# Optimization experiments

Measured on AMD Instinct MI355X. Metric: run time of the kernel, lower is better.

## Reference

```python
import jax, jax.numpy as jnp
import numpy as np

B, N, D, YD = 256, 1024, 64, 2
EPS = 1e-7  # keras SCC epsilon clip


def interleave(x):
    # (B, L, ...): out[:,0::2]=first half, out[:,1::2]=second half
    b, L = x.shape[0], x.shape[1]
    a, c = x[:, : L // 2], x[:, L // 2:]
    return jnp.stack([a, c], axis=2).reshape((b, L) + x.shape[2:])


def block_interleave(x, scope):
    # tf.split into N//scope chunks of size `scope`, Interleave each, concat
    b, L = x.shape[0], x.shape[1]
    rest = x.shape[2:]
    xr = x.reshape((b, L // scope, 2, scope // 2) + rest)
    xr = jnp.swapaxes(xr, 2, 3)
    return xr.reshape((b, L) + rest)


def split_even_odd(x):
    # returns (odd, even) = (x[:,0::2], x[:,1::2])
    return x[:, 0::2], x[:, 1::2]


def mlp2(x, W1, b1, W2, b2):
    return jnp.dot(jax.nn.relu(jnp.dot(x, W1) + b1), W2) + b2


def emb2llr(e, W, b):
    return jax.nn.softmax(jnp.dot(e, W) + b, axis=-1)


def scce(v, p):
    # v: (B,L,1) int labels, p: (B,L,2) probs -> (B,L) per-element NLL
    pt = jnp.take_along_axis(p, v, axis=-1)[..., 0]
    return -jnp.log(jnp.clip(pt, EPS, 1.0))


def setup_inputs() -> dict:
    key = jax.random.key(0)
    ks = jax.random.split(key, 16)
    s = lambda fan: 1.0 / np.sqrt(fan)
    return {
        "x": jax.random.randint(ks[0], (B, N, 1), 0, 2, dtype=jnp.int32),
        "y": jax.random.normal(ks[1], (B, N, YD), dtype=jnp.float32),
        "emb_W": jax.random.normal(ks[2], (YD, D), dtype=jnp.float32) * s(YD),
        "emb_b": jnp.zeros((D,), jnp.float32),
        "lab_emb": jax.random.normal(ks[3], (2, D), dtype=jnp.float32) * s(D),
        "cn_W1": jax.random.normal(ks[4], (2 * D, D), dtype=jnp.float32) * s(2 * D),
        "cn_b1": jnp.zeros((D,), jnp.float32),
        "cn_W2": jax.random.normal(ks[5], (D, D), dtype=jnp.float32) * s(D),
        "cn_b2": jnp.zeros((D,), jnp.float32),
        "bn_W1": jax.random.normal(ks[6], (3 * D, D), dtype=jnp.float32) * s(3 * D),
        "bn_b1": jnp.zeros((D,), jnp.float32),
        "bn_W2": jax.random.normal(ks[7], (D, D), dtype=jnp.float32) * s(D),
        "bn_b2": jnp.zeros((D,), jnp.float32),
        "llr_W": jax.random.normal(ks[8], (D, 2), dtype=jnp.float32) * s(D),
        "llr_b": jnp.zeros((2,), jnp.float32),
    }


def reference(x, y, emb_W, emb_b, lab_emb, cn_W1, cn_b1, cn_W2, cn_b2,
              bn_W1, bn_b1, bn_W2, bn_b2, llr_W, llr_b):
    v = x.astype(jnp.int32)  # (B,N,1)
    e = jnp.dot(y, emb_W) + emb_b  # (B,N,D) observation embedding

    losses, preds, norms = [], [], []
    pred = emb2llr(e, llr_W, llr_b)
    losses.append(scce(v, pred))
    preds.append(pred)
    norms.append(jnp.linalg.norm(e, axis=-1))

    scope = 2
    while scope <= N:
        v_il = block_interleave(v, scope)
        v_odd, v_even = split_even_odd(v_il)
        v_xor = jnp.mod(v_odd + v_even, 2)  # (B,N/2,1)
        v_prime = interleave(jnp.concatenate((v_xor, v_even), axis=1))

        e_il = block_interleave(e, scope)
        e_odd, e_even = split_even_odd(e_il)  # (B,N/2,D) each
        v_xor_emb = lab_emb[v_xor[..., 0]]  # (B,N/2,D)

        e1_left = mlp2(jnp.concatenate((e_odd, e_even), axis=-1),
                       cn_W1, cn_b1, cn_W2, cn_b2)
        e1_right = mlp2(jnp.concatenate((e_odd, e_even, v_xor_emb), axis=-1),
                        bn_W1, bn_b1, bn_W2, bn_b2)
        e_prime = interleave(jnp.concatenate((e1_left, e1_right), axis=1))

        pred = emb2llr(e_prime, llr_W, llr_b)
        losses.append(scce(v_prime, pred))
        preds.append(pred)
        norms.append(jnp.linalg.norm(e_prime, axis=-1))

        v, e = v_prime, e_prime
        scope *= 2

    return (jnp.stack(losses, axis=-2),   # (B, S, N)
            jnp.stack(preds, axis=-2),    # (B, N, S, 2)
            jnp.stack(norms, axis=-2))    # (B, S, N)
```

## Files before the change

kernel.cpp:

```cpp
#include <hip/hip_runtime.h>
#include <hip/hip_bf16.h>

#define NB 256
#define NN 1024
#define NSTAGES 11
#define EPSF 1e-7f

typedef unsigned short u16;
typedef unsigned int u32;
typedef unsigned long long u64;
typedef __attribute__((ext_vector_type(8))) short short8;
typedef __attribute__((ext_vector_type(16))) float f32x16;

static constexpr size_t PRED_BASE = (size_t)NB * NSTAGES * NN;
static constexpr size_t NORM_BASE = PRED_BASE + (size_t)NB * NN * NSTAGES * 2;

static constexpr int LW_OFF = 24576;

#define WLDS_FR 30
#define NWREG (48 - WLDS_FR)

__device__ __forceinline__ u16 f2bf(float f) {
  unsigned u = __float_as_uint(f);
  unsigned r = (u + 0x7fffu + ((u >> 16) & 1u)) >> 16;
  return (u16)r;
}
__device__ __forceinline__ unsigned pack_bf2(float a, float b) {
  __hip_bfloat162 h = __float22bfloat162_rn(make_float2(a, b));
  return *(unsigned*)&h;
}
__device__ __forceinline__ u32 spread16(u32 v) {
  v = (v | (v << 8)) & 0x00FF00FFu;
  v = (v | (v << 4)) & 0x0F0F0F0Fu;
  v = (v | (v << 2)) & 0x33333333u;
  v = (v | (v << 1)) & 0x55555555u;
  return v;
}
__device__ __forceinline__ void emit_out(float* __restrict__ out, int b, int n, int s,
                                         float z0, float z1, float nrm2, int label) {
  float m  = fmaxf(z0, z1);
  float p0 = expf(z0 - m), p1 = expf(z1 - m);
  float inv = 1.0f / (p0 + p1);
  p0 *= inv; p1 *= inv;
  float pt = label ? p1 : p0;
  pt = fminf(fmaxf(pt, EPSF), 1.0f);
  out[((size_t)b * NSTAGES + s) * NN + n] = -logf(pt);
  size_t pb = PRED_BASE + (((size_t)b * NN + n) * NSTAGES + s) * 2;
  out[pb + 0] = p0;
  out[pb + 1] = p1;
  out[NORM_BASE + ((size_t)b * NSTAGES + s) * NN + n] = sqrtf(nrm2);
}

__device__ __forceinline__ int eaddr(int row, int c16) {
  return row * 64 + (((c16) ^ (row & 7)) << 3);
}
__device__ __forceinline__ int eaddr32(int row, int m31) {
  return row * 64 + (((((m31) >> 2) ^ (row & 7)) << 3) | (((m31) & 3) << 1));
}

__global__ __launch_bounds__(256) void prep_kernel(
    const float* __restrict__ cn_W1, const float* __restrict__ bn_W1,
    const float* __restrict__ cn_W2, const float* __restrict__ bn_W2,
    const float* __restrict__ lab_emb, const float* __restrict__ llr_W,
    const float* __restrict__ bn_b1,
    u16* __restrict__ wfrag, float* __restrict__ labW_g) {
  int t = blockIdx.x * 256 + threadIdx.x;
  if (t < 3072) {
    int f = t >> 6, l = t & 63, h = l >> 5, c = l & 31;
    const float* src; int ks, nt;
    if (f < 16)      { src = cn_W1; ks = f >> 1; nt = f & 1; }
    else if (f < 32) { int g = f - 16; src = bn_W1; ks = g >> 1; nt = g & 1; }
    else if (f < 40) { int g = f - 32; src = cn_W2; ks = g >> 1; nt = g & 1; }
    else             { int g = f - 40; src = bn_W2; ks = g >> 1; nt = g & 1; }
    int col = 2 * c + nt;
    u16 vals[8];
    #pragma unroll
    for (int j = 0; j < 8; ++j) {
      int k = ks * 16 + h * 8 + j;
      vals[j] = f2bf(src[k * 64 + col]);
    }
    uint4 u;
    u.x = (unsigned)vals[0] | ((unsigned)vals[1] << 16);
    u.y = (unsigned)vals[2] | ((unsigned)vals[3] << 16);
    u.z = (unsigned)vals[4] | ((unsigned)vals[5] << 16);
    u.w = (unsigned)vals[6] | ((unsigned)vals[7] << 16);
    *(uint4*)(wfrag + (size_t)t * 8) = u;
  } else if (t < 3136) {
    int k = t - 3072;
    unsigned wv = (unsigned)f2bf(llr_W[k * 2]) | ((unsigned)f2bf(llr_W[k * 2 + 1]) << 16);
    ((unsigned*)(wfrag + LW_OFF))[k] = wv;
  } else if (t < 3264) {
    int idx = t - 3136;
    int v = idx >> 6, c = idx & 63;
    float acc = bn_b1[c];
    for (int d = 0; d < 64; ++d)
      acc = fmaf(lab_emb[v * 64 + d], bn_W1[(128 + d) * 64 + c], acc);
    labW_g[idx] = acc;
  }
}

#define BFR(FI) (((FI) < WLDS_FR) ? *(const short8*)(wlds + (FI) * 512 + ln * 8) \
                                  : Wreg[(FI) - WLDS_FR])

__global__ __launch_bounds__(512, 2) void polar_kernel(
    const int* __restrict__ x, const float* __restrict__ y,
    const float* __restrict__ emb_W, const float* __restrict__ emb_b,
    const u16* __restrict__ wfrag, const float* __restrict__ labW_g,
    const float* __restrict__ cn_b1, const float* __restrict__ cn_b2,
    const float* __restrict__ bn_b2, const float* __restrict__ llr_W,
    const float* __restrict__ llr_b, float* __restrict__ out) {
  __shared__ __align__(16) u16 eL[NN * 64];
  __shared__ __align__(16) u16 wlds[WLDS_FR * 512];
  __shared__ u32 lwL[64];
  __shared__ u32 vmask[2][32];
  __shared__ float labW[2][64];

  const int tid = threadIdx.x;
  const int w = tid >> 6, ln = tid & 63;
  const int m31 = ln & 31, h8 = ln >> 5;
  const int b = blockIdx.x;

  for (int i = tid; i < WLDS_FR * 64; i += 512)
    ((uint4*)wlds)[i] = ((const uint4*)wfrag)[i];
  if (tid < 64) lwL[tid] = ((const u32*)(wfrag + LW_OFF))[tid];
  if (tid < 128) ((float*)labW)[tid] = labW_g[tid];

  short8 Wreg[NWREG];
  #pragma unroll
  for (int fi = 0; fi < NWREG; ++fi)
    Wreg[fi] = *(const short8*)(wfrag + (size_t)(WLDS_FR + fi) * 512 + ln * 8);

  const float lb0 = llr_b[0], lb1 = llr_b[1];
  const float2 cb1 = *(const float2*)(cn_b1 + 2 * m31);
  const float2 cb2 = *(const float2*)(cn_b2 + 2 * m31);
  const float2 bb2 = *(const float2*)(bn_b2 + 2 * m31);

  #pragma unroll
  for (int rep = 0; rep < 2; ++rep) {
    int n = rep * 512 + tid;
    float2 yv = *(const float2*)(y + ((size_t)b * NN + n) * 2);
    float z0 = lb0, z1 = lb1, nr = 0.f;
    #pragma unroll
    for (int o8 = 0; o8 < 8; ++o8) {
      u32 vals[4];
      #pragma unroll
      for (int jj = 0; jj < 4; ++jj) {
        int o = o8 * 8 + jj * 2;
        float e0 = fmaf(yv.x, emb_W[o],     fmaf(yv.y, emb_W[64 + o],     emb_b[o]));
        float e1 = fmaf(yv.x, emb_W[o + 1], fmaf(yv.y, emb_W[64 + o + 1], emb_b[o + 1]));
        vals[jj] = pack_bf2(e0, e1);
        z0 = fmaf(e0, llr_W[o * 2 + 0], z0); z1 = fmaf(e0, llr_W[o * 2 + 1], z1);
        nr = fmaf(e0, e0, nr);
        z0 = fmaf(e1, llr_W[o * 2 + 2], z0); z1 = fmaf(e1, llr_W[o * 2 + 3], z1);
        nr = fmaf(e1, e1, nr);
      }
      uint4 q; q.x = vals[0]; q.y = vals[1]; q.z = vals[2]; q.w = vals[3];
      *(uint4*)(eL + eaddr(n, o8)) = q;
    }
    int v = x[(size_t)b * NN + n] & 1;
    emit_out(out, b, n, 0, z0, z1, nr, v);
    u64 bm = __ballot(v != 0);
    if (ln == 0)  vmask[0][rep * 16 + 2 * w]     = (u32)bm;
    if (ln == 32) vmask[0][rep * 16 + 2 * w + 1] = (u32)(bm >> 32);
  }
  __syncthreads();

  const float2 lwv0 = *(const float2*)(&labW[0][2 * m31]);
  const float2 lwv1 = *(const float2*)(&labW[1][2 * m31]);

  #pragma unroll 1
  for (int s = 1; s <= 10; ++s) {
    const int sh = s - 1;
    const int half = 1 << sh;
    const u32* vmR = vmask[(s - 1) & 1];
    u32* vmW = vmask[s & 1];

    short8 Ao[2][4], Ae[2][4];
    int io[2], ie[2], vo[2], ve[2], vx[2];
    u32 bxs[2];
    #pragma unroll
    for (int t = 0; t < 2; ++t) {
      int i = 64 * w + 32 * t + m31;
      int g = i >> sh, u = i & (half - 1);
      io[t] = g * (half << 1) + u;
      ie[t] = io[t] + half;
      #pragma unroll
      for (int f = 0; f < 4; ++f) {
        Ao[t][f] = *(const short8*)(eL + eaddr(io[t], f * 2 + h8));
        Ae[t][f] = *(const short8*)(eL + eaddr(ie[t], f * 2 + h8));
      }
      vo[t] = (vmR[io[t] >> 5] >> (io[t] & 31)) & 1;
      ve[t] = (vmR[ie[t] >> 5] >> (ie[t] & 31)) & 1;
      vx[t] = vo[t] ^ ve[t];
      u32 bx = (u32)__ballot(vx[t] != 0);
      u32 be = (u32)__ballot(ve[t] != 0);
      bxs[t] = bx;
      u32 lo = spread16(bx & 0xffffu) | (spread16(be & 0xffffu) << 1);
      u32 hi = spread16(bx >> 16) | (spread16(be >> 16) << 1);
      if (ln == 0) { vmW[4 * w + 2 * t] = lo; vmW[4 * w + 2 * t + 1] = hi; }
    }
    __syncthreads();

    if (s >= 2) {
      const uint4* lwq = (const uint4*)lwL;
      uint4 lq[4][2];
      #pragma unroll
      for (int f = 0; f < 4; ++f) {
        lq[f][0] = lwq[f * 4 + h8 * 2];
        lq[f][1] = lwq[f * 4 + h8 * 2 + 1];
      }
      #pragma unroll
      for (int t = 0; t < 2; ++t) {
        #pragma unroll
        for (int side = 0; side < 2; ++side) {
          float z0 = 0.f, z1 = 0.f, nr = 0.f;
          #pragma unroll
          for (int f = 0; f < 4; ++f) {
            short8 av8 = side ? Ae[t][f] : Ao[t][f];
            #pragma unroll
            for (int j = 0; j < 8; ++j) {
              u32 pv = ((const u32*)&av8)[j >> 1];
              float val = __uint_as_float((j & 1) ? (pv & 0xffff0000u) : (pv << 16));
              u32 lwp = (j < 4) ? ((const u32*)&lq[f][0])[j] : ((const u32*)&lq[f][1])[j - 4];
              z0 = fmaf(val, __uint_as_float(lwp << 16), z0);
              z1 = fmaf(val, __uint_as_float(lwp & 0xffff0000u), z1);
              nr = fmaf(val, val, nr);
            }
          }
          z0 += __shfl_xor(z0, 32);
          z1 += __shfl_xor(z1, 32);
          nr += __shfl_xor(nr, 32);
          if (h8 == 0)
            emit_out(out, b, side ? ie[t] : io[t], s - 1,
                     z0 + lb0, z1 + lb1, nr, side ? ve[t] : vo[t]);
        }
      }
    }

    f32x16 a0[2], a1[2];
    #pragma unroll
    for (int t = 0; t < 2; ++t)
      #pragma unroll
      for (int r = 0; r < 16; ++r) { a0[t][r] = cb1.x; a1[t][r] = cb1.y; }
    #pragma unroll
    for (int ks = 0; ks < 8; ++ks) {
      short8 B0 = BFR(ks * 2 + 0);
      short8 B1 = BFR(ks * 2 + 1);
      #pragma unroll
      for (int t = 0; t < 2; ++t) {
        short8 a = (ks < 4) ? Ao[t][ks] : Ae[t][ks - 4];
        a0[t] = __builtin_amdgcn_mfma_f32_32x32x16_bf16(a, B0, a0[t], 0, 0, 0);
        a1[t] = __builtin_amdgcn_mfma_f32_32x32x16_bf16(a, B1, a1[t], 0, 0, 0);
      }
    }
    #pragma unroll
    for (int t = 0; t < 2; ++t) {
      int obase = 128 * w + 64 * t;
      #pragma unroll
      for (int r = 0; r < 16; ++r) {
        int row = (r & 3) + 8 * (r >> 2) + 4 * h8;
        int R = obase + 2 * row;
        *(u32*)(eL + eaddr32(R, m31)) =
            pack_bf2(fmaxf(a0[t][r], 0.f), fmaxf(a1[t][r], 0.f));
      }
    }

    #pragma unroll
    for (int t = 0; t < 2; ++t)
      #pragma unroll
      for (int r = 0; r < 16; ++r) {
        int row = (r & 3) + 8 * (r >> 2) + 4 * h8;
        int bit = (bxs[t] >> row) & 1;
        a0[t][r] = bit ? lwv1.x : lwv0.x;
        a1[t][r] = bit ? lwv1.y : lwv0.y;
      }
    #pragma unroll
    for (int ks = 0; ks < 8; ++ks) {
      short8 B0 = BFR(16 + ks * 2 + 0);
      short8 B1 = BFR(16 + ks * 2 + 1);
      #pragma unroll
      for (int t = 0; t < 2; ++t) {
        short8 a = (ks < 4) ? Ao[t][ks] : Ae[t][ks - 4];
        a0[t] = __builtin_amdgcn_mfma_f32_32x32x16_bf16(a, B0, a0[t], 0, 0, 0);
        a1[t] = __builtin_amdgcn_mfma_f32_32x32x16_bf16(a, B1, a1[t], 0, 0, 0);
      }
    }
    #pragma unroll
    for (int t = 0; t < 2; ++t) {
      int obase = 128 * w + 64 * t;
      #pragma unroll
      for (int r = 0; r < 16; ++r) {
        int row = (r & 3) + 8 * (r >> 2) + 4 * h8;
        int R = obase + 2 * row + 1;
        *(u32*)(eL + eaddr32(R, m31)) =
            pack_bf2(fmaxf(a0[t][r], 0.f), fmaxf(a1[t][r], 0.f));
      }
    }

    {
      short8 Hc[2][4];
      #pragma unroll
      for (int t = 0; t < 2; ++t) {
        int R = 128 * w + 64 * t + 2 * m31;
        #pragma unroll
        for (int f = 0; f < 4; ++f)
          Hc[t][f] = *(const short8*)(eL + eaddr(R, f * 2 + h8));
      }
      f32x16 d0[2], d1[2];
      #pragma unroll
      for (int t = 0; t < 2; ++t)
        #pragma unroll
        for (int r = 0; r < 16; ++r) { d0[t][r] = cb2.x; d1[t][r] = cb2.y; }
      #pragma unroll
      for (int ks = 0; ks < 4; ++ks) {
        short8 B0 = BFR(32 + ks * 2 + 0);
        short8 B1 = BFR(32 + ks * 2 + 1);
        #pragma unroll
        for (int t = 0; t < 2; ++t) {
          d0[t] = __builtin_amdgcn_mfma_f32_32x32x16_bf16(Hc[t][ks], B0, d0[t], 0, 0, 0);
          d1[t] = __builtin_amdgcn_mfma_f32_32x32x16_bf16(Hc[t][ks], B1, d1[t], 0, 0, 0);
        }
      }
      #pragma unroll
      for (int t = 0; t < 2; ++t) {
        int obase = 128 * w + 64 * t;
        #pragma unroll
        for (int r = 0; r < 16; ++r) {
          int row = (r & 3) + 8 * (r >> 2) + 4 * h8;
          int R = obase + 2 * row;
          *(u32*)(eL + eaddr32(R, m31)) = pack_bf2(d0[t][r], d1[t][r]);
        }
      }
    }

    {
      short8 Hb[2][4];
      #pragma unroll
      for (int t = 0; t < 2; ++t) {
        int R = 128 * w + 64 * t + 2 * m31 + 1;
        #pragma unroll
        for (int f = 0; f < 4; ++f)
          Hb[t][f] = *(const short8*)(eL + eaddr(R, f * 2 + h8));
      }
      f32x16 d0[2], d1[2];
      #pragma unroll
      for (int t = 0; t < 2; ++t)
        #pragma unroll
        for (int r = 0; r < 16; ++r) { d0[t][r] = bb2.x; d1[t][r] = bb2.y; }
      #pragma unroll
      for (int ks = 0; ks < 4; ++ks) {
        short8 B0 = BFR(40 + ks * 2 + 0);
        short8 B1 = BFR(40 + ks * 2 + 1);
        #pragma unroll
        for (int t = 0; t < 2; ++t) {
          d0[t] = __builtin_amdgcn_mfma_f32_32x32x16_bf16(Hb[t][ks], B0, d0[t], 0, 0, 0);
          d1[t] = __builtin_amdgcn_mfma_f32_32x32x16_bf16(Hb[t][ks], B1, d1[t], 0, 0, 0);
        }
      }
      #pragma unroll
      for (int t = 0; t < 2; ++t) {
        int obase = 128 * w + 64 * t;
        #pragma unroll
        for (int r = 0; r < 16; ++r) {
          int row = (r & 3) + 8 * (r >> 2) + 4 * h8;
          int R = obase + 2 * row + 1;
          *(u32*)(eL + eaddr32(R, m31)) = pack_bf2(d0[t][r], d1[t][r]);
        }
      }
    }
    __syncthreads();
  }

  {
    const uint4* lwq = (const uint4*)lwL;
    uint4 lq[4][2];
    #pragma unroll
    for (int f = 0; f < 4; ++f) {
      lq[f][0] = lwq[f * 4 + h8 * 2];
      lq[f][1] = lwq[f * 4 + h8 * 2 + 1];
    }
    #pragma unroll
    for (int it = 0; it < 4; ++it) {
      int n = 128 * w + 32 * it + m31;
      float z0 = 0.f, z1 = 0.f, nr = 0.f;
      #pragma unroll
      for (int f = 0; f < 4; ++f) {
        short8 av8 = *(const short8*)(eL + eaddr(n, f * 2 + h8));
        #pragma unroll
        for (int j = 0; j < 8; ++j) {
          u32 pv = ((const u32*)&av8)[j >> 1];
          float val = __uint_as_float((j & 1) ? (pv & 0xffff0000u) : (pv << 16));
          u32 lwp = (j < 4) ? ((const u32*)&lq[f][0])[j] : ((const u32*)&lq[f][1])[j - 4];
          z0 = fmaf(val, __uint_as_float(lwp << 16), z0);
          z1 = fmaf(val, __uint_as_float(lwp & 0xffff0000u), z1);
          nr = fmaf(val, val, nr);
        }
      }
      z0 += __shfl_xor(z0, 32);
      z1 += __shfl_xor(z1, 32);
      nr += __shfl_xor(nr, 32);
      int lab = (vmask[0][n >> 5] >> (n & 31)) & 1;
      if (h8 == 0) emit_out(out, b, n, NSTAGES - 1, z0 + lb0, z1 + lb1, nr, lab);
    }
  }
}

extern "C" void kernel_launch(void* const* d_in, const int* in_sizes, int n_in,
                              void* d_out, int out_size, void* d_ws, size_t ws_size,
                              hipStream_t stream) {
  const int*   x      = (const int*)d_in[0];
  const float* y      = (const float*)d_in[1];
  const float* emb_W  = (const float*)d_in[2];
  const float* emb_b  = (const float*)d_in[3];
  const float* labemb = (const float*)d_in[4];
  const float* cn_W1  = (const float*)d_in[5];
  const float* cn_b1  = (const float*)d_in[6];
  const float* cn_W2  = (const float*)d_in[7];
  const float* cn_b2  = (const float*)d_in[8];
  const float* bn_W1  = (const float*)d_in[9];
  const float* bn_b1  = (const float*)d_in[10];
  const float* bn_W2  = (const float*)d_in[11];
  const float* bn_b2  = (const float*)d_in[12];
  const float* llr_W  = (const float*)d_in[13];
  const float* llr_b  = (const float*)d_in[14];
  float* out = (float*)d_out;

  u16* wfrag = (u16*)d_ws;
  float* labW_g = (float*)((char*)d_ws + 65536);

  prep_kernel<<<13, 256, 0, stream>>>(cn_W1, bn_W1, cn_W2, bn_W2, labemb, llr_W,
                                      bn_b1, wfrag, labW_g);
  polar_kernel<<<NB, 512, 0, stream>>>(x, y, emb_W, emb_b, wfrag, labW_g,
                                       cn_b1, cn_b2, bn_b2, llr_W, llr_b, out);
}
```

Baseline: 266.5 us.

## Stage pred outputs in LDS and workspace for coalesced transposed writes

Pred probabilities are laid out (B,N,S,2), so the old per-stage writes were strided by the stage count and poorly coalesced. Each stage's pair is now staged in an LDS buffer, copied contiguously to a global workspace, and at the end the block reloads all stages into LDS and writes the transposed layout in one coalesced pass. To make room in LDS, 8 weight fragments move from shared memory to direct global reads. The cost is extra workspace traffic, extra barriers, and weight loads through cache inside the MFMA loop. A fallback path without staging is kept for when the workspace is too small.

```diff
diff --git a/kernel.cpp b/kernel.cpp
--- a/kernel.cpp
+++ b/kernel.cpp
@@ -17,8 +17,12 @@
 
 static constexpr int LW_OFF = 24576;
 
-#define WLDS_FR 30
-#define NWREG (48 - WLDS_FR)
+#define WLDS_FR 22
+#define WGLB_END 30
+#define NWREG (48 - WGLB_END)
+
+static constexpr size_t STAGE_OFF = 131072;
+static constexpr size_t STAGE_F2_PER_B = (size_t)NSTAGES * NN;
 
 __device__ __forceinline__ u16 f2bf(float f) {
   unsigned u = __float_as_uint(f);
@@ -36,7 +40,9 @@
   v = (v | (v << 1)) & 0x55555555u;
   return v;
 }
-__device__ __forceinline__ void emit_out(float* __restrict__ out, int b, int n, int s,
+template <bool STAGED>
+__device__ __forceinline__ void emit_out(float* __restrict__ out, float* __restrict__ pstage,
+                                         int b, int n, int s,
                                          float z0, float z1, float nrm2, int label) {
   float m  = fmaxf(z0, z1);
   float p0 = expf(z0 - m), p1 = expf(z1 - m);
@@ -45,9 +51,13 @@
   float pt = label ? p1 : p0;
   pt = fminf(fmaxf(pt, EPSF), 1.0f);
   out[((size_t)b * NSTAGES + s) * NN + n] = -logf(pt);
-  size_t pb = PRED_BASE + (((size_t)b * NN + n) * NSTAGES + s) * 2;
-  out[pb + 0] = p0;
-  out[pb + 1] = p1;
+  if (STAGED) {
+    *(float2*)(pstage + 2 * n) = make_float2(p0, p1);
+  } else {
+    size_t pb = PRED_BASE + (((size_t)b * NN + n) * NSTAGES + s) * 2;
+    out[pb + 0] = p0;
+    out[pb + 1] = p1;
+  }
   out[NORM_BASE + ((size_t)b * NSTAGES + s) * NN + n] = sqrtf(nrm2);
 }
 
@@ -99,21 +109,28 @@
   }
 }
 
-#define BFR(FI) (((FI) < WLDS_FR) ? *(const short8*)(wlds + (FI) * 512 + ln * 8) \
-                                  : Wreg[(FI) - WLDS_FR])
-
+#define BFR(FI)                                                              \
+  (((FI) < WLDS_FR)                                                          \
+       ? *(const short8*)(wlds + (FI) * 512 + ln * 8)                        \
+       : (((FI) < WGLB_END)                                                  \
+              ? *(const short8*)(wfrag + (size_t)(FI) * 512 + ln * 8)        \
+              : Wreg[(FI) - WGLB_END]))
+
+template <int STAGED>
 __global__ __launch_bounds__(512, 2) void polar_kernel(
     const int* __restrict__ x, const float* __restrict__ y,
     const float* __restrict__ emb_W, const float* __restrict__ emb_b,
     const u16* __restrict__ wfrag, const float* __restrict__ labW_g,
     const float* __restrict__ cn_b1, const float* __restrict__ cn_b2,
     const float* __restrict__ bn_b2, const float* __restrict__ llr_W,
-    const float* __restrict__ llr_b, float* __restrict__ out) {
+    const float* __restrict__ llr_b, float* __restrict__ pred_ws,
+    float* __restrict__ out) {
   __shared__ __align__(16) u16 eL[NN * 64];
   __shared__ __align__(16) u16 wlds[WLDS_FR * 512];
   __shared__ u32 lwL[64];
   __shared__ u32 vmask[2][32];
   __shared__ float labW[2][64];
+  __shared__ __align__(8) float pstage[NN * 2];
 
   const int tid = threadIdx.x;
   const int w = tid >> 6, ln = tid & 63;
@@ -128,7 +145,7 @@
   short8 Wreg[NWREG];
   #pragma unroll
   for (int fi = 0; fi < NWREG; ++fi)
-    Wreg[fi] = *(const short8*)(wfrag + (size_t)(WLDS_FR + fi) * 512 + ln * 8);
+    Wreg[fi] = *(const short8*)(wfrag + (size_t)(WGLB_END + fi) * 512 + ln * 8);
 
   const float lb0 = llr_b[0], lb1 = llr_b[1];
   const float2 cb1 = *(const float2*)(cn_b1 + 2 * m31);
@@ -158,7 +175,7 @@
       *(uint4*)(eL + eaddr(n, o8)) = q;
     }
     int v = x[(size_t)b * NN + n] & 1;
-    emit_out(out, b, n, 0, z0, z1, nr, v);
+    emit_out<STAGED != 0>(out, pstage, b, n, 0, z0, z1, nr, v);
     u64 bm = __ballot(v != 0);
     if (ln == 0)  vmask[0][rep * 16 + 2 * w]     = (u32)bm;
     if (ln == 32) vmask[0][rep * 16 + 2 * w + 1] = (u32)(bm >> 32);
@@ -170,6 +187,15 @@
 
   #pragma unroll 1
   for (int s = 1; s <= 10; ++s) {
+    if (STAGED && s >= 2) {
+      float2* dstp = (float2*)pred_ws + (size_t)b * STAGE_F2_PER_B + (size_t)(s - 2) * NN;
+      #pragma unroll
+      for (int k = 0; k < 2; ++k) {
+        int i = k * 512 + tid;
+        dstp[i] = *(const float2*)(pstage + 2 * i);
+      }
+    }
+
     const int sh = s - 1;
     const int half = 1 << sh;
     const u32* vmR = vmask[(s - 1) & 1];
@@ -231,8 +257,8 @@
           z1 += __shfl_xor(z1, 32);
           nr += __shfl_xor(nr, 32);
           if (h8 == 0)
-            emit_out(out, b, side ? ie[t] : io[t], s - 1,
-                     z0 + lb0, z1 + lb1, nr, side ? ve[t] : vo[t]);
+            emit_out<STAGED != 0>(out, pstage, b, side ? ie[t] : io[t], s - 1,
+                                  z0 + lb0, z1 + lb1, nr, side ? ve[t] : vo[t]);
         }
       }
     }
@@ -367,6 +393,16 @@
           *(u32*)(eL + eaddr32(R, m31)) = pack_bf2(d0[t][r], d1[t][r]);
         }
       }
+    }
+    __syncthreads();
+  }
+
+  if (STAGED) {
+    float2* dstp = (float2*)pred_ws + (size_t)b * STAGE_F2_PER_B + (size_t)9 * NN;
+    #pragma unroll
+    for (int k = 0; k < 2; ++k) {
+      int i = k * 512 + tid;
+      dstp[i] = *(const float2*)(pstage + 2 * i);
     }
     __syncthreads();
   }
@@ -400,7 +436,24 @@
       z1 += __shfl_xor(z1, 32);
       nr += __shfl_xor(nr, 32);
       int lab = (vmask[0][n >> 5] >> (n & 31)) & 1;
-      if (h8 == 0) emit_out(out, b, n, NSTAGES - 1, z0 + lb0, z1 + lb1, nr, lab);
+      if (h8 == 0)
+        emit_out<STAGED != 0>(out, pstage, b, n, NSTAGES - 1, z0 + lb0, z1 + lb1, nr, lab);
+    }
+  }
+
+  if (STAGED) {
+    __syncthreads();
+    float2* tb = (float2*)eL;
+    const float2* src = (const float2*)pred_ws + (size_t)b * STAGE_F2_PER_B;
+    for (int i = tid; i < 10 * NN; i += 512) tb[i] = src[i];
+    for (int i = tid; i < NN; i += 512) tb[10 * NN + i] = *(const float2*)(pstage + 2 * i);
+    __syncthreads();
+    float2* dst = (float2*)(out + PRED_BASE) + (size_t)b * NN * NSTAGES;
+    #pragma unroll
+    for (int k = 0; k < 22; ++k) {
+      int lin = k * 512 + tid;
+      int n = lin / NSTAGES, sI = lin - n * NSTAGES;
+      dst[lin] = tb[sI * NN + n];
     }
   }
 }
@@ -427,9 +480,18 @@
 
   u16* wfrag = (u16*)d_ws;
   float* labW_g = (float*)((char*)d_ws + 65536);
+  float* pred_ws = (float*)((char*)d_ws + STAGE_OFF);
+  size_t need = STAGE_OFF + (size_t)NB * NSTAGES * NN * 2 * sizeof(float);
 
   prep_kernel<<<13, 256, 0, stream>>>(cn_W1, bn_W1, cn_W2, bn_W2, labemb, llr_W,
                                       bn_b1, wfrag, labW_g);
-  polar_kernel<<<NB, 512, 0, stream>>>(x, y, emb_W, emb_b, wfrag, labW_g,
-                                       cn_b1, cn_b2, bn_b2, llr_W, llr_b, out);
-}
+  if (ws_size >= need) {
+    polar_kernel<1><<<NB, 512, 0, stream>>>(x, y, emb_W, emb_b, wfrag, labW_g,
+                                            cn_b1, cn_b2, bn_b2, llr_W, llr_b,
+                                            pred_ws, out);
+  } else {
+    polar_kernel<0><<<NB, 512, 0, stream>>>(x, y, emb_W, emb_b, wfrag, labW_g,
+                                            cn_b1, cn_b2, bn_b2, llr_W, llr_b,
+                                            pred_ws, out);
+  }
+}
```

Result: slower. 290.5 us (+9.0%).

## Stage pred outputs in workspace and transpose with a separate coalescing kernel

Applied to the files above, without the earlier changes.

Prediction probabilities are written stage-major as contiguous float2 into a workspace buffer instead of strided into the final (B,N,S,2) layout. A new kernel then transposes each batch row through shared memory into the required layout with coalesced writes. This aims to cut the cost of scattered global stores in the main kernel. In exchange it adds an extra global read/write pass and a kernel launch, and it only takes this path when the workspace is large enough.

```diff
diff --git a/kernel.cpp b/kernel.cpp
--- a/kernel.cpp
+++ b/kernel.cpp
@@ -19,6 +19,9 @@
 
 #define WLDS_FR 30
 #define NWREG (48 - WLDS_FR)
+
+static constexpr size_t STAGE_OFF = 131072;
+static constexpr size_t PRED_F2_PER_B = (size_t)NSTAGES * NN;
 
 __device__ __forceinline__ u16 f2bf(float f) {
   unsigned u = __float_as_uint(f);
@@ -36,7 +39,9 @@
   v = (v | (v << 1)) & 0x55555555u;
   return v;
 }
-__device__ __forceinline__ void emit_out(float* __restrict__ out, int b, int n, int s,
+template <bool STAGED>
+__device__ __forceinline__ void emit_out(float* __restrict__ out, float* __restrict__ pred_ws,
+                                         int b, int n, int s,
                                          float z0, float z1, float nrm2, int label) {
   float m  = fmaxf(z0, z1);
   float p0 = expf(z0 - m), p1 = expf(z1 - m);
@@ -45,9 +50,13 @@
   float pt = label ? p1 : p0;
   pt = fminf(fmaxf(pt, EPSF), 1.0f);
   out[((size_t)b * NSTAGES + s) * NN + n] = -logf(pt);
-  size_t pb = PRED_BASE + (((size_t)b * NN + n) * NSTAGES + s) * 2;
-  out[pb + 0] = p0;
-  out[pb + 1] = p1;
+  if (STAGED) {
+    ((float2*)pred_ws)[((size_t)b * NSTAGES + s) * NN + n] = make_float2(p0, p1);
+  } else {
+    size_t pb = PRED_BASE + (((size_t)b * NN + n) * NSTAGES + s) * 2;
+    out[pb + 0] = p0;
+    out[pb + 1] = p1;
+  }
   out[NORM_BASE + ((size_t)b * NSTAGES + s) * NN + n] = sqrtf(nrm2);
 }
 
@@ -99,16 +108,36 @@
   }
 }
 
+__global__ __launch_bounds__(512) void pred_transpose_kernel(
+    const float* __restrict__ pred_ws, float* __restrict__ out) {
+  __shared__ float2 tb[NSTAGES * 1026];
+  const int tid = threadIdx.x;
+  const int b = blockIdx.x;
+  const float2* src = (const float2*)pred_ws + (size_t)b * PRED_F2_PER_B;
+  for (int i = tid; i < NSTAGES * NN; i += 512) {
+    int s = i >> 10, n = i & (NN - 1);
+    tb[s * 1026 + n] = src[i];
+  }
+  __syncthreads();
+  float2* dst = (float2*)(out + PRED_BASE) + (size_t)b * PRED_F2_PER_B;
+  for (int j = tid; j < NSTAGES * NN; j += 512) {
+    int n = j / NSTAGES, s = j - n * NSTAGES;
+    dst[j] = tb[s * 1026 + n];
+  }
+}
+
 #define BFR(FI) (((FI) < WLDS_FR) ? *(const short8*)(wlds + (FI) * 512 + ln * 8) \
                                   : Wreg[(FI) - WLDS_FR])
 
+template <int STAGED>
 __global__ __launch_bounds__(512, 2) void polar_kernel(
     const int* __restrict__ x, const float* __restrict__ y,
     const float* __restrict__ emb_W, const float* __restrict__ emb_b,
     const u16* __restrict__ wfrag, const float* __restrict__ labW_g,
     const float* __restrict__ cn_b1, const float* __restrict__ cn_b2,
     const float* __restrict__ bn_b2, const float* __restrict__ llr_W,
-    const float* __restrict__ llr_b, float* __restrict__ out) {
+    const float* __restrict__ llr_b, float* __restrict__ pred_ws,
+    float* __restrict__ out) {
   __shared__ __align__(16) u16 eL[NN * 64];
   __shared__ __align__(16) u16 wlds[WLDS_FR * 512];
   __shared__ u32 lwL[64];
@@ -158,7 +187,7 @@
       *(uint4*)(eL + eaddr(n, o8)) = q;
     }
     int v = x[(size_t)b * NN + n] & 1;
-    emit_out(out, b, n, 0, z0, z1, nr, v);
+    emit_out<STAGED != 0>(out, pred_ws, b, n, 0, z0, z1, nr, v);
     u64 bm = __ballot(v != 0);
     if (ln == 0)  vmask[0][rep * 16 + 2 * w]     = (u32)bm;
     if (ln == 32) vmask[0][rep * 16 + 2 * w + 1] = (u32)(bm >> 32);
@@ -231,8 +260,8 @@
           z1 += __shfl_xor(z1, 32);
           nr += __shfl_xor(nr, 32);
           if (h8 == 0)
-            emit_out(out, b, side ? ie[t] : io[t], s - 1,
-                     z0 + lb0, z1 + lb1, nr, side ? ve[t] : vo[t]);
+            emit_out<STAGED != 0>(out, pred_ws, b, side ? ie[t] : io[t], s - 1,
+                                  z0 + lb0, z1 + lb1, nr, side ? ve[t] : vo[t]);
         }
       }
     }
@@ -400,7 +429,8 @@
       z1 += __shfl_xor(z1, 32);
       nr += __shfl_xor(nr, 32);
       int lab = (vmask[0][n >> 5] >> (n & 31)) & 1;
-      if (h8 == 0) emit_out(out, b, n, NSTAGES - 1, z0 + lb0, z1 + lb1, nr, lab);
+      if (h8 == 0)
+        emit_out<STAGED != 0>(out, pred_ws, b, n, NSTAGES - 1, z0 + lb0, z1 + lb1, nr, lab);
     }
   }
 }
@@ -427,9 +457,19 @@
 
   u16* wfrag = (u16*)d_ws;
   float* labW_g = (float*)((char*)d_ws + 65536);
+  float* pred_ws = (float*)((char*)d_ws + STAGE_OFF);
+  size_t need = STAGE_OFF + (size_t)NB * NSTAGES * NN * 2 * sizeof(float);
 
   prep_kernel<<<13, 256, 0, stream>>>(cn_W1, bn_W1, cn_W2, bn_W2, labemb, llr_W,
                                       bn_b1, wfrag, labW_g);
-  polar_kernel<<<NB, 512, 0, stream>>>(x, y, emb_W, emb_b, wfrag, labW_g,
-                                       cn_b1, cn_b2, bn_b2, llr_W, llr_b, out);
-}
+  if (ws_size >= need) {
+    polar_kernel<1><<<NB, 512, 0, stream>>>(x, y, emb_W, emb_b, wfrag, labW_g,
+                                            cn_b1, cn_b2, bn_b2, llr_W, llr_b,
+                                            pred_ws, out);
+    pred_transpose_kernel<<<NB, 512, 0, stream>>>(pred_ws, out);
+  } else {
+    polar_kernel<0><<<NB, 512, 0, stream>>>(x, y, emb_W, emb_b, wfrag, labW_g,
+                                            cn_b1, cn_b2, bn_b2, llr_W, llr_b,
+                                            pred_ws, out);
+  }
+}
```

New measurement: 265.2 us. About the same (-0.5%).
